# Optimization experiments

Hardware: AMD Instinct MI355X
Metric: run time of the kernel (lower is better)

## Reference

```python
import jax, jax.numpy as jnp
import numpy as np

NUM_HEADS = 12
HEAD_DIM = 64
LMBDA = 0.01
BLIND_SPOT = True


def setup_inputs() -> dict:
    key = jax.random.key(0)
    ks = jax.random.split(key, 4)
    B, S, D = 8, 1024, 768
    scale = 1.0 / np.sqrt(D)
    return {
        "hidden_states": jax.random.normal(ks[0], (B, S, D), jnp.float32),
        "attention_mask": jnp.zeros((B, 1, 1, S), jnp.float32),
        "Wq": jax.random.normal(ks[1], (D, D), jnp.float32) * scale,
        "bq": jnp.zeros((D,), jnp.float32),
        "Wk": jax.random.normal(ks[2], (D, D), jnp.float32) * scale,
        "bk": jnp.zeros((D,), jnp.float32),
        "Wv": jax.random.normal(ks[3], (D, D), jnp.float32) * scale,
        "bv": jnp.zeros((D,), jnp.float32),
    }


def _split_heads(x):
    B, S, D = x.shape
    return x.reshape(B, S, NUM_HEADS, HEAD_DIM).transpose(0, 2, 1, 3)  # [B,H,S,dh]


def reference(hidden_states, attention_mask, Wq, bq, Wk, bk, Wv, bv):
    B, S, D = hidden_states.shape
    q = _split_heads(hidden_states @ Wq + bq)
    k = _split_heads(hidden_states @ Wk + bk)
    v = _split_heads(hidden_states @ Wv + bv)

    scores = jnp.einsum("bhqd,bhkd->bhqk", q, k)  # [B,H,S,S]
    if BLIND_SPOT:
        # zero out the diagonal BEFORE scaling (matches original order)
        eye = jnp.eye(S, dtype=scores.dtype)
        scores = scores * (1.0 - eye)
    scores = scores / np.sqrt(HEAD_Dim() if False else HEAD_DIM).astype(np.float32)
    scores = scores + attention_mask  # additive mask, broadcast [B,1,1,S]

    # auxiliary diagonal-weighted regularization loss
    if LMBDA != 0.0:
        diag_vals = jnp.diagonal(scores, axis1=-2, axis2=-1)  # [B,H,S]
        loss = LMBDA * jnp.sum(diag_vals)
    else:
        loss = jnp.float32(0.0)

    probs = jax.nn.softmax(scores, axis=-1)  # dropout = identity (eval)
    context = jnp.einsum("bhqk,bhkd->bhqd", probs, v)  # [B,H,S,dh]
    context = context.transpose(0, 2, 1, 3).reshape(B, S, D)
    return context, loss
```

## Files before the change

kernel.cpp:

```cpp
#include <hip/hip_runtime.h>
#include <hip/hip_bf16.h>
#include <stdint.h>

#define Bb 8
#define Ss 1024
#define Dd 768
#define Hh 12
#define DH 64

typedef __attribute__((ext_vector_type(8))) short bf16x8;
typedef __attribute__((ext_vector_type(4))) float f32x4;

static __device__ __forceinline__ unsigned short f2b(float x) {
    union { float f; unsigned u; } v; v.f = x;
    unsigned r = v.u + 0x7FFFu + ((v.u >> 16) & 1u);
    return (unsigned short)(r >> 16);
}

static __device__ __forceinline__ void gll16(const void* g, void* l) {
    __builtin_amdgcn_global_load_lds((const __attribute__((address_space(1))) void*)g,
                                     (__attribute__((address_space(3))) void*)l,
                                     16, 0, 0);
}

__global__ __launch_bounds__(256) void k_cvt(const float* __restrict__ in,
                                             unsigned short* __restrict__ out) {
    int i = (blockIdx.x * 256 + threadIdx.x) * 4;
    const float4 v = *reinterpret_cast<const float4*>(in + i);
    ushort4 o;
    o.x = f2b(v.x); o.y = f2b(v.y); o.z = f2b(v.z); o.w = f2b(v.w);
    *reinterpret_cast<ushort4*>(out + i) = o;
}

__global__ __launch_bounds__(256) void k_twt(const float* __restrict__ Wq,
                                             const float* __restrict__ Wk,
                                             const float* __restrict__ Wv,
                                             unsigned short* __restrict__ Wt) {
    __shared__ float tile[32][33];
    const int w = blockIdx.z;
    const float* W = (w == 0) ? Wq : (w == 1) ? Wk : Wv;
    const int k0 = blockIdx.x * 32, n0 = blockIdx.y * 32;
    const int c = threadIdx.x & 31, r0 = threadIdx.x >> 5;
    #pragma unroll
    for (int i = 0; i < 4; ++i)
        tile[r0 + i * 8][c] = W[(size_t)(k0 + r0 + i * 8) * Dd + n0 + c];
    __syncthreads();
    unsigned short* o = Wt + (size_t)w * Dd * Dd;
    #pragma unroll
    for (int i = 0; i < 4; ++i)
        o[(size_t)(n0 + r0 + i * 8) * Dd + k0 + c] = f2b(tile[c][r0 + i * 8]);
}

__global__ __launch_bounds__(256) void k_qkv(
    const unsigned short* __restrict__ hb,
    const unsigned short* __restrict__ Wt,
    const float* __restrict__ bq, const float* __restrict__ bk, const float* __restrict__ bv,
    unsigned short* __restrict__ Qo, unsigned short* __restrict__ Ko,
    unsigned short* __restrict__ Vo) {
    __shared__ __align__(16) unsigned short Al[128 * 32];
    __shared__ __align__(16) unsigned short Bl[128 * 32];
    const int m0 = blockIdx.x * 128;
    const int n0 = blockIdx.y * 128;
    const int w  = blockIdx.z;
    const int tid = threadIdx.x, lane = tid & 63, wv = tid >> 6;
    const int l15 = lane & 15, l4 = lane >> 4;
    const int wm = (wv >> 1) * 64, wn = (wv & 1) * 64;
    const unsigned short* Wb = Wt + (size_t)w * Dd * Dd;

    f32x4 acc[4][4];
    #pragma unroll
    for (int i = 0; i < 4; ++i)
        #pragma unroll
        for (int j = 0; j < 4; ++j)
            acc[i][j] = f32x4{0.f, 0.f, 0.f, 0.f};

    const int ldr = lane >> 2;
    const int ldc = (lane & 3) * 8;

    for (int kt = 0; kt < Dd / 32; ++kt) {
        const int k0 = kt * 32;
        #pragma unroll
        for (int i = 0; i < 2; ++i) {
            const int c = wv * 2 + i;
            gll16(hb + (size_t)(m0 + c * 16 + ldr) * Dd + k0 + ldc, Al + c * 512);
            gll16(Wb + (size_t)(n0 + c * 16 + ldr) * Dd + k0 + ldc, Bl + c * 512);
        }
        __syncthreads();
        bf16x8 af[4], bfr[4];
        #pragma unroll
        for (int i = 0; i < 4; ++i) {
            af[i]  = *reinterpret_cast<const bf16x8*>(Al + (wm + i * 16 + l15) * 32 + l4 * 8);
            bfr[i] = *reinterpret_cast<const bf16x8*>(Bl + (wn + i * 16 + l15) * 32 + l4 * 8);
        }
        #pragma unroll
        for (int i = 0; i < 4; ++i)
            #pragma unroll
            for (int j = 0; j < 4; ++j)
                acc[i][j] = __builtin_amdgcn_mfma_f32_16x16x32_bf16(af[i], bfr[j], acc[i][j], 0, 0, 0);
        __syncthreads();
    }

    const float* bias = (w == 0) ? bq : (w == 1) ? bk : bv;
    if (w < 2) {
        unsigned short* O = (w == 0) ? Qo : Ko;
        #pragma unroll
        for (int j = 0; j < 4; ++j) {
            const int n = n0 + wn + j * 16 + l15;
            const float bs = bias[n];
            const int hh = n >> 6, d = n & 63;
            #pragma unroll
            for (int i = 0; i < 4; ++i) {
                const int mb = m0 + wm + i * 16 + l4 * 4;
                #pragma unroll
                for (int r = 0; r < 4; ++r) {
                    const int m = mb + r;
                    const int b = m >> 10, s = m & 1023;
                    O[(((size_t)b * Hh + hh) * Ss + s) * DH + d] = f2b(acc[i][j][r] + bs);
                }
            }
        }
    } else {
        #pragma unroll
        for (int j = 0; j < 4; ++j) {
            const int n = n0 + wn + j * 16 + l15;
            const float bs = bias[n];
            const int hh = n >> 6, d = n & 63;
            #pragma unroll
            for (int i = 0; i < 4; ++i) {
                const int m = m0 + wm + i * 16 + l4 * 4;
                const int b = m >> 10, s = m & 1023;
                ushort4 o;
                o.x = f2b(acc[i][j][0] + bs);
                o.y = f2b(acc[i][j][1] + bs);
                o.z = f2b(acc[i][j][2] + bs);
                o.w = f2b(acc[i][j][3] + bs);
                *reinterpret_cast<ushort4*>(Vo + (((size_t)b * Hh + hh) * DH + d) * Ss + s) = o;
            }
        }
    }
}

__global__ __launch_bounds__(256) void k_attn(
    const unsigned short* __restrict__ Q,
    const unsigned short* __restrict__ K,
    const unsigned short* __restrict__ VT,
    const float* __restrict__ mask,
    float* __restrict__ out) {
    __shared__ __align__(16) unsigned short Kl[64 * 64];
    __shared__ __align__(16) unsigned short Vl[64 * 64];
    __shared__ __align__(16) unsigned short Pl[4][16][72];
    __shared__ __align__(16) float Ml[1024];

    const int bid = blockIdx.x;
    const int wg  = (bid & 7) * 192 + (bid >> 3);
    const int bh  = wg >> 4;
    const int qt  = wg & 15;
    const int b = bh / Hh, h = bh % Hh;
    const int tid = threadIdx.x, lane = tid & 63, wv = tid >> 6;
    const int l15 = lane & 15, l4 = lane >> 4;
    const int q0 = qt * 64 + wv * 16;

    const unsigned short* Qb = Q + (size_t)bh * Ss * DH;
    const unsigned short* Kb = K + (size_t)bh * Ss * DH;
    const unsigned short* Vb = VT + (size_t)bh * DH * Ss;
    const float* mb = mask + (size_t)b * Ss;

    {
        const float4 mv = *reinterpret_cast<const float4*>(mb + tid * 4);
        float4 ms;
        ms.x = mv.x * 1.44269504f; ms.y = mv.y * 1.44269504f;
        ms.z = mv.z * 1.44269504f; ms.w = mv.w * 1.44269504f;
        *reinterpret_cast<float4*>(&Ml[tid * 4]) = ms;
    }

    const bf16x8 qf0 = *reinterpret_cast<const bf16x8*>(Qb + (q0 + l15) * DH + l4 * 8);
    const bf16x8 qf1 = *reinterpret_cast<const bf16x8*>(Qb + (q0 + l15) * DH + 32 + l4 * 8);

    float m2 = -3.0e38f, lsum = 0.f;
    f32x4 oacc[4];
    #pragma unroll
    for (int dt = 0; dt < 4; ++dt) oacc[dt] = f32x4{0.f, 0.f, 0.f, 0.f};

    const float C1 = 0.125f * 1.44269504f;

    const int srow = lane >> 3;
    const int sslt = lane & 7;

    for (int kt = 0; kt < Ss / 64; ++kt) {
        {
            const int r0 = wv * 16;
            #pragma unroll
            for (int i = 0; i < 2; ++i) {
                const int rK = r0 + i * 8 + srow;
                const int gsK = sslt ^ (rK & 7);
                gll16(Kb + (size_t)(kt * 64 + rK) * DH + gsK * 8, Kl + (r0 + i * 8) * 64);
                gll16(Vb + (size_t)rK * Ss + kt * 64 + gsK * 8,   Vl + (r0 + i * 8) * 64);
            }
        }
        __syncthreads();

        f32x4 sc[4];
        #pragma unroll
        for (int ct = 0; ct < 4; ++ct) {
            const int kr = ct * 16 + l15;
            const int sw = kr & 7;
            const bf16x8 kf0 = *reinterpret_cast<const bf16x8*>(Kl + kr * 64 + ((l4 ^ sw) * 8));
            const bf16x8 kf1 = *reinterpret_cast<const bf16x8*>(Kl + kr * 64 + (((l4 + 4) ^ sw) * 8));
            f32x4 a = f32x4{0.f, 0.f, 0.f, 0.f};
            a = __builtin_amdgcn_mfma_f32_16x16x32_bf16(kf0, qf0, a, 0, 0, 0);
            a = __builtin_amdgcn_mfma_f32_16x16x32_bf16(kf1, qf1, a, 0, 0, 0);
            sc[ct] = a;
        }

        float4 mk[4];
        #pragma unroll
        for (int ct = 0; ct < 4; ++ct)
            mk[ct] = *reinterpret_cast<const float4*>(&Ml[kt * 64 + ct * 16 + l4 * 4]);

        float p[16];
        float pmax = -3.0e38f;
        const bool dk = (kt == qt);
        #pragma unroll
        for (int ct = 0; ct < 4; ++ct) {
            const float* mkp = reinterpret_cast<const float*>(&mk[ct]);
            #pragma unroll
            for (int r = 0; r < 4; ++r) {
                float t = fmaf(sc[ct][r], C1, mkp[r]);
                if (dk && (ct * 16 + l4 * 4 + r) == (wv * 16 + l15)) t = mkp[r];
                p[ct * 4 + r] = t;
                pmax = fmaxf(pmax, t);
            }
        }
        pmax = fmaxf(pmax, __shfl_xor(pmax, 16));
        pmax = fmaxf(pmax, __shfl_xor(pmax, 32));

        if (__any(pmax > m2 + 10.f)) {
            const float mnew = fmaxf(m2, pmax);
            const float alpha = __builtin_amdgcn_exp2f(m2 - mnew);
            m2 = mnew;
            lsum *= alpha;
            float ar[4];
            #pragma unroll
            for (int r = 0; r < 4; ++r) ar[r] = __shfl(alpha, l4 * 4 + r);
            #pragma unroll
            for (int dt = 0; dt < 4; ++dt)
                #pragma unroll
                for (int r = 0; r < 4; ++r) oacc[dt][r] *= ar[r];
        }

        float rs = 0.f;
        #pragma unroll
        for (int i = 0; i < 16; ++i) {
            const float e = __builtin_amdgcn_exp2f(p[i] - m2);
            p[i] = e;
            rs += e;
        }
        rs += __shfl_xor(rs, 16);
        rs += __shfl_xor(rs, 32);
        lsum += rs;

        #pragma unroll
        for (int ct = 0; ct < 4; ++ct) {
            unsigned lo, hi;
            asm("v_cvt_pk_bf16_f32 %0, %1, %2" : "=v"(lo) : "v"(p[ct * 4 + 0]), "v"(p[ct * 4 + 1]));
            asm("v_cvt_pk_bf16_f32 %0, %1, %2" : "=v"(hi) : "v"(p[ct * 4 + 2]), "v"(p[ct * 4 + 3]));
            *reinterpret_cast<uint2*>(&Pl[wv][l15][ct * 16 + l4 * 4]) = make_uint2(lo, hi);
        }

        const bf16x8 pf0 = *reinterpret_cast<const bf16x8*>(&Pl[wv][l15][l4 * 8]);
        const bf16x8 pf1 = *reinterpret_cast<const bf16x8*>(&Pl[wv][l15][32 + l4 * 8]);
        #pragma unroll
        for (int dt = 0; dt < 4; ++dt) {
            const int vr = dt * 16 + l15;
            const int sv = vr & 7;
            const bf16x8 vf0 = *reinterpret_cast<const bf16x8*>(Vl + vr * 64 + ((l4 ^ sv) * 8));
            const bf16x8 vf1 = *reinterpret_cast<const bf16x8*>(Vl + vr * 64 + (((l4 + 4) ^ sv) * 8));
            oacc[dt] = __builtin_amdgcn_mfma_f32_16x16x32_bf16(pf0, vf0, oacc[dt], 0, 0, 0);
            oacc[dt] = __builtin_amdgcn_mfma_f32_16x16x32_bf16(pf1, vf1, oacc[dt], 0, 0, 0);
        }
        __syncthreads();
    }

    #pragma unroll
    for (int r = 0; r < 4; ++r) {
        const float li = __shfl(lsum, l4 * 4 + r);
        const float inv = 1.f / li;
        const int s = qt * 64 + wv * 16 + l4 * 4 + r;
        float* op = out + ((size_t)b * Ss + s) * Dd + h * DH;
        #pragma unroll
        for (int dt = 0; dt < 4; ++dt)
            op[dt * 16 + l15] = oacc[dt][r] * inv;
    }
}

__global__ __launch_bounds__(256) void k_loss(const float* __restrict__ mask,
                                              float* __restrict__ out) {
    __shared__ float red[4];
    float s = 0.f;
    for (int i = threadIdx.x; i < Bb * Ss; i += 256) s += mask[i];
    #pragma unroll
    for (int d = 1; d < 64; d <<= 1) s += __shfl_xor(s, d);
    const int lane = threadIdx.x & 63, wv = threadIdx.x >> 6;
    if (lane == 0) red[wv] = s;
    __syncthreads();
    if (threadIdx.x == 0)
        out[0] = 0.01f * 12.f * (red[0] + red[1] + red[2] + red[3]);
}

extern "C" void kernel_launch(void* const* d_in, const int* in_sizes, int n_in,
                              void* d_out, int out_size, void* d_ws, size_t ws_size,
                              hipStream_t stream) {
    const float* hs   = (const float*)d_in[0];
    const float* mask = (const float*)d_in[1];
    const float* Wq   = (const float*)d_in[2];
    const float* bq   = (const float*)d_in[3];
    const float* Wk   = (const float*)d_in[4];
    const float* bk   = (const float*)d_in[5];
    const float* Wv   = (const float*)d_in[6];
    const float* bv   = (const float*)d_in[7];
    float* out = (float*)d_out;

    uint8_t* ws = (uint8_t*)d_ws;
    unsigned short* hb = (unsigned short*)(ws);
    unsigned short* Wt = (unsigned short*)(ws + 12582912);
    unsigned short* Qw = (unsigned short*)(ws + 16121856);
    unsigned short* Kw = (unsigned short*)(ws + 28704768);
    unsigned short* Vw = (unsigned short*)(ws + 41287680);

    hipLaunchKernelGGL(k_cvt,  dim3(6144),      dim3(256), 0, stream, hs, hb);
    hipLaunchKernelGGL(k_twt,  dim3(24, 24, 3), dim3(256), 0, stream, Wq, Wk, Wv, Wt);
    hipLaunchKernelGGL(k_qkv,  dim3(64, 6, 3),  dim3(256), 0, stream, hb, Wt, bq, bk, bv, Qw, Kw, Vw);
    hipLaunchKernelGGL(k_attn, dim3(1536),      dim3(256), 0, stream, Qw, Kw, Vw, mask, out);
    hipLaunchKernelGGL(k_loss, dim3(1),         dim3(256), 0, stream, mask, out + 6291456);
}
```

Measured before the change: 211.0 us.

## Merge prep kernels, double-buffer QKV GEMM loads, and swizzle block order

Three preprocessing kernels (hidden-state bf16 conversion, weight transpose and loss reduction) are merged into one launch, which removes two kernel launches. The QKV GEMM now uses double-buffered LDS so the next K tile is loaded while the current one is computed, with one barrier per iteration instead of two. The GEMM grid is flattened with a grouped block ordering to improve L2 reuse of A and W tiles. This doubles LDS use per block and changes how blocks are assigned to tiles.

Result: no change. 215.2 us (+2.0%).

```diff
diff --git a/kernel.cpp b/kernel.cpp
--- a/kernel.cpp
+++ b/kernel.cpp
@@ -23,32 +23,47 @@
                                      16, 0, 0);
 }
 
-__global__ __launch_bounds__(256) void k_cvt(const float* __restrict__ in,
-                                             unsigned short* __restrict__ out) {
-    int i = (blockIdx.x * 256 + threadIdx.x) * 4;
-    const float4 v = *reinterpret_cast<const float4*>(in + i);
-    ushort4 o;
-    o.x = f2b(v.x); o.y = f2b(v.y); o.z = f2b(v.z); o.w = f2b(v.w);
-    *reinterpret_cast<ushort4*>(out + i) = o;
-}
-
-__global__ __launch_bounds__(256) void k_twt(const float* __restrict__ Wq,
-                                             const float* __restrict__ Wk,
-                                             const float* __restrict__ Wv,
-                                             unsigned short* __restrict__ Wt) {
+__global__ __launch_bounds__(256) void k_prep(
+    const float* __restrict__ hs,
+    const float* __restrict__ Wq, const float* __restrict__ Wk, const float* __restrict__ Wv,
+    const float* __restrict__ mask,
+    unsigned short* __restrict__ hb, unsigned short* __restrict__ Wt,
+    float* __restrict__ loss_out) {
     __shared__ float tile[32][33];
-    const int w = blockIdx.z;
-    const float* W = (w == 0) ? Wq : (w == 1) ? Wk : Wv;
-    const int k0 = blockIdx.x * 32, n0 = blockIdx.y * 32;
-    const int c = threadIdx.x & 31, r0 = threadIdx.x >> 5;
-    #pragma unroll
-    for (int i = 0; i < 4; ++i)
-        tile[r0 + i * 8][c] = W[(size_t)(k0 + r0 + i * 8) * Dd + n0 + c];
-    __syncthreads();
-    unsigned short* o = Wt + (size_t)w * Dd * Dd;
-    #pragma unroll
-    for (int i = 0; i < 4; ++i)
-        o[(size_t)(n0 + r0 + i * 8) * Dd + k0 + c] = f2b(tile[c][r0 + i * 8]);
+    __shared__ float red[4];
+    const int bid = blockIdx.x;
+    const int tid = threadIdx.x;
+    if (bid < 6144) {
+        const int i = (bid * 256 + tid) * 4;
+        const float4 v = *reinterpret_cast<const float4*>(hs + i);
+        ushort4 o;
+        o.x = f2b(v.x); o.y = f2b(v.y); o.z = f2b(v.z); o.w = f2b(v.w);
+        *reinterpret_cast<ushort4*>(hb + i) = o;
+    } else if (bid < 7872) {
+        const int t = bid - 6144;
+        const int w = t / 576, rem = t % 576;
+        const int k0 = (rem / 24) * 32, n0 = (rem % 24) * 32;
+        const float* W = (w == 0) ? Wq : (w == 1) ? Wk : Wv;
+        const int c = tid & 31, r0 = tid >> 5;
+        #pragma unroll
+        for (int i = 0; i < 4; ++i)
+            tile[r0 + i * 8][c] = W[(size_t)(k0 + r0 + i * 8) * Dd + n0 + c];
+        __syncthreads();
+        unsigned short* o = Wt + (size_t)w * Dd * Dd;
+        #pragma unroll
+        for (int i = 0; i < 4; ++i)
+            o[(size_t)(n0 + r0 + i * 8) * Dd + k0 + c] = f2b(tile[c][r0 + i * 8]);
+    } else {
+        float s = 0.f;
+        for (int i = tid; i < Bb * Ss; i += 256) s += mask[i];
+        #pragma unroll
+        for (int d = 1; d < 64; d <<= 1) s += __shfl_xor(s, d);
+        const int lane = tid & 63, wv = tid >> 6;
+        if (lane == 0) red[wv] = s;
+        __syncthreads();
+        if (tid == 0)
+            loss_out[0] = 0.01f * 12.f * (red[0] + red[1] + red[2] + red[3]);
+    }
 }
 
 __global__ __launch_bounds__(256) void k_qkv(
@@ -57,15 +72,17 @@
     const float* __restrict__ bq, const float* __restrict__ bk, const float* __restrict__ bv,
     unsigned short* __restrict__ Qo, unsigned short* __restrict__ Ko,
     unsigned short* __restrict__ Vo) {
-    __shared__ __align__(16) unsigned short Al[128 * 32];
-    __shared__ __align__(16) unsigned short Bl[128 * 32];
-    const int m0 = blockIdx.x * 128;
-    const int n0 = blockIdx.y * 128;
-    const int w  = blockIdx.z;
+    __shared__ __align__(16) unsigned short Al[2][4096];
+    __shared__ __align__(16) unsigned short Bl[2][4096];
+    const int bid = blockIdx.x;
+    const int x = bid & 7, local = bid >> 3;
+    const int mt = x * 8 + (local & 7);
+    const int nt = local >> 3;
+    const int m0 = mt * 128, n0 = nt * 128;
+    const int w  = nt / 6;
     const int tid = threadIdx.x, lane = tid & 63, wv = tid >> 6;
     const int l15 = lane & 15, l4 = lane >> 4;
     const int wm = (wv >> 1) * 64, wn = (wv & 1) * 64;
-    const unsigned short* Wb = Wt + (size_t)w * Dd * Dd;
 
     f32x4 acc[4][4];
     #pragma unroll
@@ -77,37 +94,53 @@
     const int ldr = lane >> 2;
     const int ldc = (lane & 3) * 8;
 
-    for (int kt = 0; kt < Dd / 32; ++kt) {
-        const int k0 = kt * 32;
-        #pragma unroll
-        for (int i = 0; i < 2; ++i) {
-            const int c = wv * 2 + i;
-            gll16(hb + (size_t)(m0 + c * 16 + ldr) * Dd + k0 + ldc, Al + c * 512);
-            gll16(Wb + (size_t)(n0 + c * 16 + ldr) * Dd + k0 + ldc, Bl + c * 512);
-        }
-        __syncthreads();
-        bf16x8 af[4], bfr[4];
-        #pragma unroll
-        for (int i = 0; i < 4; ++i) {
-            af[i]  = *reinterpret_cast<const bf16x8*>(Al + (wm + i * 16 + l15) * 32 + l4 * 8);
-            bfr[i] = *reinterpret_cast<const bf16x8*>(Bl + (wn + i * 16 + l15) * 32 + l4 * 8);
-        }
-        #pragma unroll
-        for (int i = 0; i < 4; ++i)
-            #pragma unroll
-            for (int j = 0; j < 4; ++j)
-                acc[i][j] = __builtin_amdgcn_mfma_f32_16x16x32_bf16(af[i], bfr[j], acc[i][j], 0, 0, 0);
-        __syncthreads();
-    }
+    #define STAGE(buf, kt)                                                              \
+        {                                                                               \
+            const int k0_ = (kt) * 32;                                                  \
+            _Pragma("unroll")                                                           \
+            for (int i_ = 0; i_ < 2; ++i_) {                                            \
+                const int c_ = wv * 2 + i_;                                             \
+                gll16(hb + (size_t)(m0 + c_ * 16 + ldr) * Dd + k0_ + ldc, &Al[buf][c_ * 512]); \
+                gll16(Wt + (size_t)(n0 + c_ * 16 + ldr) * Dd + k0_ + ldc, &Bl[buf][c_ * 512]); \
+            }                                                                           \
+        }
+
+    #define COMPUTE(buf)                                                                \
+        {                                                                               \
+            bf16x8 af_[4], bf_[4];                                                      \
+            _Pragma("unroll")                                                           \
+            for (int i_ = 0; i_ < 4; ++i_) {                                            \
+                af_[i_] = *reinterpret_cast<const bf16x8*>(&Al[buf][(wm + i_ * 16 + l15) * 32 + l4 * 8]); \
+                bf_[i_] = *reinterpret_cast<const bf16x8*>(&Bl[buf][(wn + i_ * 16 + l15) * 32 + l4 * 8]); \
+            }                                                                           \
+            _Pragma("unroll")                                                           \
+            for (int i_ = 0; i_ < 4; ++i_)                                              \
+                _Pragma("unroll")                                                       \
+                for (int j_ = 0; j_ < 4; ++j_)                                          \
+                    acc[i_][j_] = __builtin_amdgcn_mfma_f32_16x16x32_bf16(af_[i_], bf_[j_], acc[i_][j_], 0, 0, 0); \
+        }
+
+    STAGE(0, 0);
+    __syncthreads();
+    int buf = 0;
+    for (int kt = 1; kt < Dd / 32; ++kt) {
+        STAGE(buf ^ 1, kt);
+        COMPUTE(buf);
+        __syncthreads();
+        buf ^= 1;
+    }
+    COMPUTE(buf);
+    #undef STAGE
+    #undef COMPUTE
 
     const float* bias = (w == 0) ? bq : (w == 1) ? bk : bv;
     if (w < 2) {
         unsigned short* O = (w == 0) ? Qo : Ko;
         #pragma unroll
         for (int j = 0; j < 4; ++j) {
-            const int n = n0 + wn + j * 16 + l15;
-            const float bs = bias[n];
-            const int hh = n >> 6, d = n & 63;
+            const int nL = n0 + wn + j * 16 + l15 - w * Dd;
+            const float bs = bias[nL];
+            const int hh = nL >> 6, d = nL & 63;
             #pragma unroll
             for (int i = 0; i < 4; ++i) {
                 const int mb = m0 + wm + i * 16 + l4 * 4;
@@ -122,9 +155,9 @@
     } else {
         #pragma unroll
         for (int j = 0; j < 4; ++j) {
-            const int n = n0 + wn + j * 16 + l15;
-            const float bs = bias[n];
-            const int hh = n >> 6, d = n & 63;
+            const int nL = n0 + wn + j * 16 + l15 - 2 * Dd;
+            const float bs = bias[nL];
+            const int hh = nL >> 6, d = nL & 63;
             #pragma unroll
             for (int i = 0; i < 4; ++i) {
                 const int m = m0 + wm + i * 16 + l4 * 4;
@@ -291,20 +324,6 @@
         for (int dt = 0; dt < 4; ++dt)
             op[dt * 16 + l15] = oacc[dt][r] * inv;
     }
-}
-
-__global__ __launch_bounds__(256) void k_loss(const float* __restrict__ mask,
-                                              float* __restrict__ out) {
-    __shared__ float red[4];
-    float s = 0.f;
-    for (int i = threadIdx.x; i < Bb * Ss; i += 256) s += mask[i];
-    #pragma unroll
-    for (int d = 1; d < 64; d <<= 1) s += __shfl_xor(s, d);
-    const int lane = threadIdx.x & 63, wv = threadIdx.x >> 6;
-    if (lane == 0) red[wv] = s;
-    __syncthreads();
-    if (threadIdx.x == 0)
-        out[0] = 0.01f * 12.f * (red[0] + red[1] + red[2] + red[3]);
 }
 
 extern "C" void kernel_launch(void* const* d_in, const int* in_sizes, int n_in,
@@ -327,9 +346,9 @@
     unsigned short* Kw = (unsigned short*)(ws + 28704768);
     unsigned short* Vw = (unsigned short*)(ws + 41287680);
 
-    hipLaunchKernelGGL(k_cvt,  dim3(6144),      dim3(256), 0, stream, hs, hb);
-    hipLaunchKernelGGL(k_twt,  dim3(24, 24, 3), dim3(256), 0, stream, Wq, Wk, Wv, Wt);
-    hipLaunchKernelGGL(k_qkv,  dim3(64, 6, 3),  dim3(256), 0, stream, hb, Wt, bq, bk, bv, Qw, Kw, Vw);
-    hipLaunchKernelGGL(k_attn, dim3(1536),      dim3(256), 0, stream, Qw, Kw, Vw, mask, out);
-    hipLaunchKernelGGL(k_loss, dim3(1),         dim3(256), 0, stream, mask, out + 6291456);
-}
+    hipLaunchKernelGGL(k_prep, dim3(7873), dim3(256), 0, stream,
+                       hs, Wq, Wk, Wv, mask, hb, Wt, out + 6291456);
+    hipLaunchKernelGGL(k_qkv,  dim3(1152), dim3(256), 0, stream,
+                       hb, Wt, bq, bk, bv, Qw, Kw, Vw);
+    hipLaunchKernelGGL(k_attn, dim3(1536), dim3(256), 0, stream, Qw, Kw, Vw, mask, out);
+}
```
